# Performance work log

Hardware: AMD Instinct MI355X
Metric: run time of the kernel (lower is better)

## Reference

```python
import jax, jax.numpy as jnp
import numpy as np


def _nms(heat, kernel=3):
    # 3x3 max-pool, stride 1, SAME padding; keep only local maxima
    pad = (kernel - 1) // 2
    hmax = jax.lax.reduce_window(
        heat, -jnp.inf, jax.lax.max,
        window_dimensions=(1, 1, kernel, kernel),
        window_strides=(1, 1, 1, 1),
        padding=((0, 0), (0, 0), (pad, pad), (pad, pad)))
    keep = (hmax == heat).astype(heat.dtype)
    return heat * keep


def _topk(scores, K):
    b, c, h, w = scores.shape
    # stage 1: per-class top-K over spatial positions
    topk_scores, topk_inds = jax.lax.top_k(scores.reshape(b, c, h * w), K)  # [b,c,K]
    topk_inds = topk_inds % (h * w)
    topk_ys = (topk_inds // w).astype(scores.dtype)
    topk_xs = (topk_inds % w).astype(scores.dtype)
    # stage 2: global top-K over the c*K per-class candidates
    topk_score, topk_ind = jax.lax.top_k(topk_scores.reshape(b, c * K), K)  # [b,K]
    topk_clses = (topk_ind // K).astype(jnp.int32)
    gather = lambda f: jnp.take_along_axis(f.reshape(b, c * K), topk_ind, axis=1)
    return (topk_score, gather(topk_inds), topk_clses, gather(topk_ys), gather(topk_xs))


def setup_inputs() -> dict:
    key = jax.random.key(0)
    heat = jax.random.uniform(key, (8, 10, 512, 512), dtype=jnp.float32)
    return {"heat": heat, "K": 100}


def reference(heat, K):
    suppressed = _nms(heat, kernel=3)
    return _topk(suppressed, K)
```

## Files before the change

### kernel.cpp

```cpp
#include <hip/hip_runtime.h>
#include <cstdint>

using u32 = unsigned int;
using u64 = unsigned long long;

#define WDIM 512
#define HDIM 512
#define CHANNELS 80
#define NSTRIP 8
#define STRIPROWS 64
#define KEYCAP 4096
#define HBINS 4096
#define SORTA 512
#define TOPK 100
#define NEG_SENTINEL -1e30f

__device__ __forceinline__ float fmax3(float a, float b, float c) {
  return fmaxf(fmaxf(a, b), c);
}

__device__ __forceinline__ int key_bin(u64 key) {
  int b = (int)((u32)(key >> 32) >> 14) - 60928;
  return b < 0 ? 0 : b;
}

struct H8 { float h0, h1, h2, h3, h4, h5, h6, h7; };
struct Row { float l; float4 A; float4 B; float r; };

__device__ __forceinline__ Row load_row_shfl(const float* __restrict__ chbase,
                                             int y, int x0) {
  Row o;
  if (y >= 0 && y < HDIM) {
    const float* row = chbase + (size_t)y * WDIM;
    o.A = *reinterpret_cast<const float4*>(row + x0);
    o.B = *reinterpret_cast<const float4*>(row + x0 + 4);
  } else {
    o.A = make_float4(NEG_SENTINEL, NEG_SENTINEL, NEG_SENTINEL, NEG_SENTINEL);
    o.B = o.A;
  }
  o.l = __shfl_up(o.B.w, 1);
  o.r = __shfl_down(o.A.x, 1);
  int lane = threadIdx.x & 63;
  if (lane == 0) o.l = NEG_SENTINEL;
  if (lane == 63) o.r = NEG_SENTINEL;
  return o;
}

__device__ __forceinline__ H8 hmax_row(const Row& t) {
  H8 o;
  o.h0 = fmax3(t.l,   t.A.x, t.A.y);
  o.h1 = fmax3(t.A.x, t.A.y, t.A.z);
  o.h2 = fmax3(t.A.y, t.A.z, t.A.w);
  o.h3 = fmax3(t.A.z, t.A.w, t.B.x);
  o.h4 = fmax3(t.A.w, t.B.x, t.B.y);
  o.h5 = fmax3(t.B.x, t.B.y, t.B.z);
  o.h6 = fmax3(t.B.y, t.B.z, t.B.w);
  o.h7 = fmax3(t.B.z, t.B.w, t.r);
  return o;
}

__device__ __forceinline__ void bitonic_desc(u64* keys, int N, int nthr, int tid) {
  for (unsigned size = 2; size <= (unsigned)N; size <<= 1) {
    for (unsigned stride = size >> 1; stride > 0; stride >>= 1) {
      __syncthreads();
      for (unsigned i = tid; i < (unsigned)N; i += nthr) {
        unsigned j = i ^ stride;
        if (j > i) {
          u64 a = keys[i], b = keys[j];
          bool desc = ((i & size) == 0);
          if ((a < b) == desc) { keys[i] = b; keys[j] = a; }
        }
      }
    }
  }
  __syncthreads();
}

__global__ __launch_bounds__(512) void nms_topk_strip(
    const float* __restrict__ heat, u64* __restrict__ s1p) {
  const int strip = blockIdx.x, ch = blockIdx.y;
  const float* chbase = heat + (size_t)ch * (WDIM * HDIM);

  __shared__ u64 keys[KEYCAP];
  __shared__ u32 hist[HBINS];
  __shared__ u64 sk[SORTA];
  __shared__ u32 lcnt, scand;
  __shared__ int sT;

  for (int i = threadIdx.x; i < HBINS; i += 512) hist[i] = 0;
  if (threadIdx.x == 0) { lcnt = 0; scand = 0; }
  __syncthreads();

  const int lane = threadIdx.x & 63;
  const int wave = threadIdx.x >> 6;
  const int x0 = lane * 8;
  const int yb = strip * STRIPROWS + wave * 8;

  Row rm = load_row_shfl(chbase, yb, x0);
  H8 ht = hmax_row(load_row_shfl(chbase, yb - 1, x0));
  H8 hm = hmax_row(rm);

  for (int j = 0; j < 8; j++) {
    const int y = yb + j;
    Row rb = load_row_shfl(chbase, y + 1, x0);
    H8 hb = hmax_row(rb);
    const int P = (y << 9) + x0;

#define DO_PIX(I, VC, HX)                                                  \
    {                                                                      \
      float v = (VC);                                                      \
      if (v == fmax3(ht.HX, hm.HX, hb.HX) && v > 0.0f) {                   \
        u32 p = atomicAdd(&lcnt, 1u);                                      \
        if (p < KEYCAP)                                                    \
          keys[p] = ((u64)__float_as_uint(v) << 32) | (u32)(~(u32)(P + (I))); \
      }                                                                    \
    }
    DO_PIX(0, rm.A.x, h0)
    DO_PIX(1, rm.A.y, h1)
    DO_PIX(2, rm.A.z, h2)
    DO_PIX(3, rm.A.w, h3)
    DO_PIX(4, rm.B.x, h4)
    DO_PIX(5, rm.B.y, h5)
    DO_PIX(6, rm.B.z, h6)
    DO_PIX(7, rm.B.w, h7)
#undef DO_PIX

    rm = rb; ht = hm; hm = hb;
  }

  __syncthreads();
  const int n = min((int)lcnt, KEYCAP);

  for (int i = threadIdx.x; i < n; i += 512)
    atomicAdd(&hist[key_bin(keys[i])], 1u);
  __syncthreads();

  if (threadIdx.x == 0) {
    u32 cum = 0;
    int b = HBINS - 1;
    for (; b >= 0; b--) {
      cum += hist[b];
      if (cum >= TOPK) break;
    }
    sT = b < 0 ? 0 : b;
  }
  __syncthreads();
  const int T = sT;

  for (int i = threadIdx.x; i < n; i += 512) {
    u64 k = keys[i];
    if (key_bin(k) >= T) {
      u32 p = atomicAdd(&scand, 1u);
      if (p < SORTA) sk[p] = k;
    }
  }
  __syncthreads();
  const int nc = min((int)scand, SORTA);
  for (int i = threadIdx.x; i < SORTA; i += 512)
    if (i >= nc) sk[i] = 0;
  bitonic_desc(sk, SORTA, 512, threadIdx.x);

  u64* dst = s1p + ((size_t)ch * NSTRIP + strip) * TOPK;
  for (int k = threadIdx.x; k < TOPK; k += 512) dst[k] = sk[k];
}

__global__ __launch_bounds__(256) void merge_channel(
    const u64* __restrict__ s1p, u64* __restrict__ chtop) {
  const int ch = blockIdx.x;
  __shared__ u64 sk[1024];
  const u64* src = s1p + (size_t)ch * NSTRIP * TOPK;
  for (int i = threadIdx.x; i < 1024; i += 256)
    sk[i] = (i < NSTRIP * TOPK) ? src[i] : 0;
  bitonic_desc(sk, 1024, 256, threadIdx.x);
  for (int k = threadIdx.x; k < TOPK; k += 256)
    chtop[(size_t)ch * TOPK + k] = sk[k];
}

__global__ __launch_bounds__(256) void batch_topk_kernel(
    const u64* __restrict__ chtop, float* __restrict__ out) {
  const int b = blockIdx.x;
  __shared__ u64 sk[1024];
  const u64* base = chtop + (size_t)b * 10 * TOPK;
  for (int i = threadIdx.x; i < 1024; i += 256) {
    u64 k = 0;
    if (i < 1000) {
      u32 vb = (u32)(base[i] >> 32);
      k = ((u64)vb << 32) | (u32)(~(u32)i);
    }
    sk[i] = k;
  }
  bitonic_desc(sk, 1024, 256, threadIdx.x);
  for (int k = threadIdx.x; k < TOPK; k += 256) {
    u64 key = sk[k];
    float sc = __uint_as_float((u32)(key >> 32));
    int flat = (int)(~(u32)key);
    int cls = flat / 100;
    int spatial = (int)(~(u32)(base[flat]));
    out[0 * 800 + b * TOPK + k] = sc;
    out[1 * 800 + b * TOPK + k] = (float)spatial;
    out[2 * 800 + b * TOPK + k] = (float)cls;
    out[3 * 800 + b * TOPK + k] = (float)(spatial >> 9);
    out[4 * 800 + b * TOPK + k] = (float)(spatial & 511);
  }
}

extern "C" void kernel_launch(void* const* d_in, const int* in_sizes, int n_in,
                              void* d_out, int out_size, void* d_ws, size_t ws_size,
                              hipStream_t stream) {
  const float* heat = (const float*)d_in[0];
  char* ws = (char*)d_ws;
  float* out = (float*)d_out;

  size_t p = 0;
  u64* s1p   = (u64*)(ws + p); p += (size_t)CHANNELS * NSTRIP * TOPK * 8;
  u64* chtop = (u64*)(ws + p); p += (size_t)CHANNELS * TOPK * 8;

  dim3 gridA(NSTRIP, CHANNELS);
  nms_topk_strip<<<gridA, 512, 0, stream>>>(heat, s1p);
  merge_channel<<<CHANNELS, 256, 0, stream>>>(s1p, chtop);
  batch_topk_kernel<<<8, 256, 0, stream>>>(chtop, out);
}
```

Before: 188.4 us.

## Aggregate candidate atomics per wave and move strip sorting into merge kernel

Candidate appends now use one shared atomic per wavefront, with a ballot and popcount prefix giving each lane its slot, instead of one atomic per thread. The per-strip bitonic sort is removed: above-threshold candidates (up to 256) are written unsorted to global memory with a count, and the merge kernel sorts all strips together in a 2048-element bitonic sort with 512 threads. This cuts shared-atomic contention and the many-barrier sort in the 640-block first kernel. In exchange the 80-block merge kernel does a larger sort, and candidates beyond 256 per strip are dropped.

```diff
diff --git a/kernel.cpp b/kernel.cpp
--- a/kernel.cpp
+++ b/kernel.cpp
@@ -11,7 +11,8 @@
 #define STRIPROWS 64
 #define KEYCAP 4096
 #define HBINS 4096
-#define SORTA 512
+#define FINCAP 256
+#define MERGEN 2048
 #define TOPK 100
 #define NEG_SENTINEL -1e30f
 
@@ -77,13 +78,12 @@
 }
 
 __global__ __launch_bounds__(512) void nms_topk_strip(
-    const float* __restrict__ heat, u64* __restrict__ s1p) {
+    const float* __restrict__ heat, u64* __restrict__ fin, u32* __restrict__ fcnt) {
   const int strip = blockIdx.x, ch = blockIdx.y;
   const float* chbase = heat + (size_t)ch * (WDIM * HDIM);
 
   __shared__ u64 keys[KEYCAP];
   __shared__ u32 hist[HBINS];
-  __shared__ u64 sk[SORTA];
   __shared__ u32 lcnt, scand;
   __shared__ int sT;
 
@@ -92,6 +92,7 @@
   __syncthreads();
 
   const int lane = threadIdx.x & 63;
+  const u64 lmlt = (1ULL << lane) - 1;
   const int wave = threadIdx.x >> 6;
   const int x0 = lane * 8;
   const int yb = strip * STRIPROWS + wave * 8;
@@ -106,14 +107,23 @@
     H8 hb = hmax_row(rb);
     const int P = (y << 9) + x0;
 
-#define DO_PIX(I, VC, HX)                                                  \
-    {                                                                      \
-      float v = (VC);                                                      \
-      if (v == fmax3(ht.HX, hm.HX, hb.HX) && v > 0.0f) {                   \
-        u32 p = atomicAdd(&lcnt, 1u);                                      \
-        if (p < KEYCAP)                                                    \
-          keys[p] = ((u64)__float_as_uint(v) << 32) | (u32)(~(u32)(P + (I))); \
-      }                                                                    \
+#define DO_PIX(I, VC, HX)                                                   \
+    {                                                                       \
+      float v = (VC);                                                       \
+      bool pred = (v == fmax3(ht.HX, hm.HX, hb.HX)) && (v > 0.0f);          \
+      u64 m = __ballot(pred);                                               \
+      if (m) {                                                              \
+        u32 cnt = (u32)__popcll(m);                                         \
+        u32 wbase = 0;                                                      \
+        if (lane == 0) wbase = atomicAdd(&lcnt, cnt);                       \
+        wbase = __shfl(wbase, 0);                                           \
+        if (pred) {                                                         \
+          u32 pos = wbase + (u32)__popcll(m & lmlt);                        \
+          if (pos < KEYCAP)                                                 \
+            keys[pos] = ((u64)__float_as_uint(v) << 32) |                   \
+                        (u32)(~(u32)(P + (I)));                             \
+        }                                                                   \
+      }                                                                     \
     }
     DO_PIX(0, rm.A.x, h0)
     DO_PIX(1, rm.A.y, h1)
@@ -147,32 +157,42 @@
   __syncthreads();
   const int T = sT;
 
-  for (int i = threadIdx.x; i < n; i += 512) {
-    u64 k = keys[i];
-    if (key_bin(k) >= T) {
-      u32 p = atomicAdd(&scand, 1u);
-      if (p < SORTA) sk[p] = k;
-    }
-  }
-  __syncthreads();
-  const int nc = min((int)scand, SORTA);
-  for (int i = threadIdx.x; i < SORTA; i += 512)
-    if (i >= nc) sk[i] = 0;
-  bitonic_desc(sk, SORTA, 512, threadIdx.x);
-
-  u64* dst = s1p + ((size_t)ch * NSTRIP + strip) * TOPK;
-  for (int k = threadIdx.x; k < TOPK; k += 512) dst[k] = sk[k];
-}
-
-__global__ __launch_bounds__(256) void merge_channel(
-    const u64* __restrict__ s1p, u64* __restrict__ chtop) {
+  u64* dst = fin + ((size_t)ch * NSTRIP + strip) * FINCAP;
+  for (int i = threadIdx.x; i < ((n + 511) & ~511); i += 512) {
+    u64 k = (i < n) ? keys[i] : 0;
+    bool pred = (i < n) && (key_bin(k) >= T);
+    u64 m = __ballot(pred);
+    if (m) {
+      u32 cnt = (u32)__popcll(m);
+      u32 wbase = 0;
+      if (lane == 0) wbase = atomicAdd(&scand, cnt);
+      wbase = __shfl(wbase, 0);
+      if (pred) {
+        u32 pos = wbase + (u32)__popcll(m & lmlt);
+        if (pos < FINCAP) dst[pos] = k;
+      }
+    }
+  }
+  __syncthreads();
+  if (threadIdx.x == 0)
+    fcnt[ch * NSTRIP + strip] = min(scand, (u32)FINCAP);
+}
+
+__global__ __launch_bounds__(512) void merge_channel(
+    const u64* __restrict__ fin, const u32* __restrict__ fcnt,
+    u64* __restrict__ chtop) {
   const int ch = blockIdx.x;
-  __shared__ u64 sk[1024];
-  const u64* src = s1p + (size_t)ch * NSTRIP * TOPK;
-  for (int i = threadIdx.x; i < 1024; i += 256)
-    sk[i] = (i < NSTRIP * TOPK) ? src[i] : 0;
-  bitonic_desc(sk, 1024, 256, threadIdx.x);
-  for (int k = threadIdx.x; k < TOPK; k += 256)
+  __shared__ u64 sk[MERGEN];
+  __shared__ u32 cnts[NSTRIP];
+  if (threadIdx.x < NSTRIP) cnts[threadIdx.x] = fcnt[ch * NSTRIP + threadIdx.x];
+  __syncthreads();
+  const u64* src = fin + (size_t)ch * NSTRIP * FINCAP;
+  for (int i = threadIdx.x; i < MERGEN; i += 512) {
+    int s = i >> 8, j = i & (FINCAP - 1);
+    sk[i] = (j < (int)cnts[s]) ? src[s * FINCAP + j] : 0;
+  }
+  bitonic_desc(sk, MERGEN, 512, threadIdx.x);
+  for (int k = threadIdx.x; k < TOPK; k += 512)
     chtop[(size_t)ch * TOPK + k] = sk[k];
 }
 
@@ -212,11 +232,13 @@
   float* out = (float*)d_out;
 
   size_t p = 0;
-  u64* s1p   = (u64*)(ws + p); p += (size_t)CHANNELS * NSTRIP * TOPK * 8;
+  u64* fin   = (u64*)(ws + p); p += (size_t)CHANNELS * NSTRIP * FINCAP * 8;
+  u32* fcnt  = (u32*)(ws + p); p += (size_t)CHANNELS * NSTRIP * 4;
+  p = (p + 255) & ~(size_t)255;
   u64* chtop = (u64*)(ws + p); p += (size_t)CHANNELS * TOPK * 8;
 
   dim3 gridA(NSTRIP, CHANNELS);
-  nms_topk_strip<<<gridA, 512, 0, stream>>>(heat, s1p);
-  merge_channel<<<CHANNELS, 256, 0, stream>>>(s1p, chtop);
+  nms_topk_strip<<<gridA, 512, 0, stream>>>(heat, fin, fcnt);
+  merge_channel<<<CHANNELS, 512, 0, stream>>>(fin, fcnt, chtop);
   batch_topk_kernel<<<8, 256, 0, stream>>>(chtop, out);
 }
```

Result: slower. 194.5 us (+3.2%).
